# Performance work log

Hardware: AMD Instinct MI355X
Metric: run time of the kernel (lower is better)

## Reference

```python
import jax, jax.numpy as jnp
import numpy as np

EMBED = 1024
HEADS = 16
HEAD_DIM = EMBED // HEADS
MAX_REL = 8
B, S = 4, 1024


def setup_inputs() -> dict:
    key = jax.random.key(0)
    ks = jax.random.split(key, 12)
    lim = 1.0 / np.sqrt(EMBED)
    def lin(k):
        k1, k2 = jax.random.split(k)
        W = jax.random.uniform(k1, (EMBED, EMBED), jnp.float32, -lim, lim)
        b = jax.random.uniform(k2, (EMBED,), jnp.float32, -lim, lim)
        return W, b
    Wq, bq = lin(ks[0]); Wk, bk = lin(ks[1]); Wv, bv = lin(ks[2]); Wo, bo = lin(ks[3])
    return {
        'query': jax.random.normal(ks[4], (B, S, EMBED), jnp.float32),
        'key': jax.random.normal(ks[5], (B, S, EMBED), jnp.float32),
        'value': jax.random.normal(ks[6], (B, S, EMBED), jnp.float32),
        'mask': jnp.zeros((B, S, S), dtype=bool),
        'Wq': Wq, 'bq': bq, 'Wk': Wk, 'bk': bk, 'Wv': Wv, 'bv': bv,
        'Wo': Wo, 'bo': bo,
        'rel_bias': jnp.zeros((HEADS, 2 * MAX_REL + 1), jnp.float32),
    }


def _split_heads(x):
    b, s, _ = x.shape
    return x.reshape(b, s, HEADS, HEAD_DIM).transpose(0, 2, 1, 3)  # [b,h,s,d]


def reference(query, key, value, mask, Wq, bq, Wk, bk, Wv, bv, Wo, bo, rel_bias):
    scale = jnp.sqrt(jnp.float32(HEAD_DIM))
    Q = _split_heads(query @ Wq.T + bq)
    K = _split_heads(key @ Wk.T + bk)
    V = _split_heads(value @ Wv.T + bv)
    scores = jnp.einsum('bhqd,bhkd->bhqk', Q, K) / scale
    # relative position bias: rel_bias[h, clip(j-i)+max]
    idx = jnp.arange(query.shape[1])
    rel = jnp.clip(idx[None, :] - idx[:, None], -MAX_REL, MAX_REL) + MAX_REL  # [s,s]
    bias = rel_bias[:, rel]  # [h,s,s]
    scores = scores + bias[None]
    scores = jnp.where(mask[:, None, :, :], -jnp.inf, scores)
    attn = jax.nn.softmax(scores, axis=-1)
    ctx = jnp.einsum('bhqk,bhkd->bhqd', attn, V)
    b, h, s, d = ctx.shape
    out = ctx.transpose(0, 2, 1, 3).reshape(b, s, h * d) @ Wo.T + bo
    return out, attn, scores
```

## Files before the change

### kernel.cpp

```cpp
#include <hip/hip_runtime.h>

typedef __bf16 bf16_t;
typedef bf16_t bf16x4 __attribute__((ext_vector_type(4)));
typedef bf16_t bf16x8 __attribute__((ext_vector_type(8)));
typedef float f32x4 __attribute__((ext_vector_type(4)));
typedef float f32x8 __attribute__((ext_vector_type(8)));

#define B_N 4
#define S_N 1024
#define E_N 1024
#define H_N 16
#define D_N 64

#define MFMA16 __builtin_amdgcn_mfma_f32_16x16x32_bf16

static __device__ __forceinline__ bf16_t f2b(float x) { return (bf16_t)x; }

static __device__ __forceinline__ void gload_lds16(const void* g, void* l) {
  __builtin_amdgcn_global_load_lds(
      (const __attribute__((address_space(1))) unsigned int*)g,
      (__attribute__((address_space(3))) unsigned int*)l, 16, 0, 0);
}

static __device__ __forceinline__ void lds_barrier() {
  asm volatile("s_waitcnt lgkmcnt(0)\n\ts_barrier" ::: "memory");
  __builtin_amdgcn_sched_barrier(0);
}

__global__ __launch_bounds__(256) void convert_kernel(
    const float* __restrict__ q, const float* __restrict__ k, const float* __restrict__ v,
    const float* __restrict__ wq, const float* __restrict__ wk,
    const float* __restrict__ wv, const float* __restrict__ wo,
    bf16_t* __restrict__ dq, bf16_t* __restrict__ dk, bf16_t* __restrict__ dv,
    bf16_t* __restrict__ dwq, bf16_t* __restrict__ dwk,
    bf16_t* __restrict__ dwv, bf16_t* __restrict__ dwo)
{
  const size_t e = ((size_t)blockIdx.x * 256 + threadIdx.x) * 8;
  const float* src; bf16_t* dst; size_t off;
  if (e < 12582912ull) {
    const int which = (int)(e >> 22);
    off = e & 4194303ull;
    src = which == 0 ? q : (which == 1 ? k : v);
    dst = which == 0 ? dq : (which == 1 ? dk : dv);
  } else {
    const size_t e2 = e - 12582912ull;
    const int which = (int)(e2 >> 20);
    off = e2 & 1048575ull;
    src = which == 0 ? wq : (which == 1 ? wk : (which == 2 ? wv : wo));
    dst = which == 0 ? dwq : (which == 1 ? dwk : (which == 2 ? dwv : dwo));
  }
  f32x8 x = *(const f32x8*)(src + off);
  bf16x8 r;
#pragma unroll
  for (int i = 0; i < 8; ++i) r[i] = f2b(x[i]);
  *(bf16x8*)(dst + off) = r;
}

__global__ __launch_bounds__(256) void mask_rowany(
    const unsigned char* __restrict__ mask, unsigned char* __restrict__ flags)
{
  const int row = blockIdx.x * 4 + (threadIdx.x >> 6);
  const int lane = threadIdx.x & 63;
  const uint4 v = *(const uint4*)(mask + (size_t)row * 1024 + lane * 16);
  const unsigned int any = v.x | v.y | v.z | v.w;
  const unsigned long long bal = __ballot(any != 0);
  if (lane == 0) flags[row] = bal ? 1 : 0;
}

__global__ __launch_bounds__(256) void qkv_gemm(
    const bf16_t* __restrict__ qA, const bf16_t* __restrict__ kA, const bf16_t* __restrict__ vA,
    const bf16_t* __restrict__ Wq, const bf16_t* __restrict__ Wk, const bf16_t* __restrict__ Wv,
    const float* __restrict__ bq, const float* __restrict__ bk, const float* __restrict__ bv,
    bf16_t* __restrict__ Qo, bf16_t* __restrict__ Ko, bf16_t* __restrict__ Vto)
{
  const int z = blockIdx.z;
  const bf16_t* A = z == 0 ? qA : (z == 1 ? kA : vA);
  const bf16_t* W = z == 0 ? Wq : (z == 1 ? Wk : Wv);
  const float* bias = z == 0 ? bq : (z == 1 ? bk : bv);

  __shared__ bf16_t As[128 * 32];
  __shared__ bf16_t Bs[128 * 32];
  const int tid = threadIdx.x;
  const int m0 = blockIdx.y * 128, n0 = blockIdx.x * 128;
  const int lane = tid & 63, wid = tid >> 6;
  const int wr = wid >> 1, wc = wid & 1;
  const int lr = lane & 15, lh = lane >> 4;
  const int sr = lane >> 2, sc = (lane & 3) * 8;
  f32x4 acc[4][4] = {};
  for (int k0 = 0; k0 < 1024; k0 += 32) {
#pragma unroll
    for (int i = 0; i < 2; ++i) {
      const int br = wid * 32 + i * 16;
      gload_lds16(&A[(size_t)(m0 + br + sr) * 1024 + k0 + sc], &As[br * 32]);
      gload_lds16(&W[(size_t)(n0 + br + sr) * 1024 + k0 + sc], &Bs[br * 32]);
    }
    __syncthreads();
    bf16x8 af[4], bw[4];
#pragma unroll
    for (int m = 0; m < 4; ++m)
      af[m] = *(const bf16x8*)&As[(wr * 64 + m * 16 + lr) * 32 + lh * 8];
#pragma unroll
    for (int n = 0; n < 4; ++n)
      bw[n] = *(const bf16x8*)&Bs[(wc * 64 + n * 16 + lr) * 32 + lh * 8];
#pragma unroll
    for (int m = 0; m < 4; ++m)
#pragma unroll
      for (int n = 0; n < 4; ++n)
        acc[m][n] = MFMA16(af[m], bw[n], acc[m][n], 0, 0, 0);
    __syncthreads();
  }
#pragma unroll
  for (int n = 0; n < 4; ++n) {
    const int col = n0 + wc * 64 + n * 16 + lr;
    const float bv_ = bias[col];
    const int h = col >> 6, d = col & 63;
#pragma unroll
    for (int m = 0; m < 4; ++m) {
      const int row0 = m0 + wr * 64 + m * 16 + lh * 4;
#pragma unroll
      for (int r = 0; r < 4; ++r) {
        const int row = row0 + r;
        const float v = acc[m][n][r] + bv_;
        const int b = row >> 10, s = row & 1023;
        if (z == 0)
          Qo[((size_t)(b * H_N + h) * S_N + s) * D_N + d] = f2b(v);
        else if (z == 1)
          Ko[((size_t)(b * H_N + h) * S_N + s) * D_N + d] = f2b(v);
        else
          Vto[((size_t)(b * H_N + h) * D_N + d) * S_N + s] = f2b(v);
      }
    }
  }
}

__global__ __launch_bounds__(256) void out_gemm(
    const bf16_t* __restrict__ A, const bf16_t* __restrict__ W,
    const float* __restrict__ bias, float* __restrict__ Co)
{
  __shared__ bf16_t As[128 * 32];
  __shared__ bf16_t Bs[128 * 32];
  const int tid = threadIdx.x;
  const int m0 = blockIdx.y * 128, n0 = blockIdx.x * 128;
  const int lane = tid & 63, wid = tid >> 6;
  const int wr = wid >> 1, wc = wid & 1;
  const int lr = lane & 15, lh = lane >> 4;
  const int sr = lane >> 2, sc = (lane & 3) * 8;
  f32x4 acc[4][4] = {};
  for (int k0 = 0; k0 < 1024; k0 += 32) {
#pragma unroll
    for (int i = 0; i < 2; ++i) {
      const int br = wid * 32 + i * 16;
      gload_lds16(&A[(size_t)(m0 + br + sr) * 1024 + k0 + sc], &As[br * 32]);
      gload_lds16(&W[(size_t)(n0 + br + sr) * 1024 + k0 + sc], &Bs[br * 32]);
    }
    __syncthreads();
    bf16x8 af[4], bw[4];
#pragma unroll
    for (int m = 0; m < 4; ++m)
      af[m] = *(const bf16x8*)&As[(wr * 64 + m * 16 + lr) * 32 + lh * 8];
#pragma unroll
    for (int n = 0; n < 4; ++n)
      bw[n] = *(const bf16x8*)&Bs[(wc * 64 + n * 16 + lr) * 32 + lh * 8];
#pragma unroll
    for (int m = 0; m < 4; ++m)
#pragma unroll
      for (int n = 0; n < 4; ++n)
        acc[m][n] = MFMA16(af[m], bw[n], acc[m][n], 0, 0, 0);
    __syncthreads();
  }
#pragma unroll
  for (int n = 0; n < 4; ++n) {
    const int col = n0 + wc * 64 + n * 16 + lr;
    const float bv_ = bias[col];
#pragma unroll
    for (int m = 0; m < 4; ++m) {
      const int row0 = m0 + wr * 64 + m * 16 + lh * 4;
#pragma unroll
      for (int r = 0; r < 4; ++r)
        Co[(size_t)(row0 + r) * E_N + col] = acc[m][n][r] + bv_;
    }
  }
}

static __device__ __forceinline__ f32x4 score4(
    f32x4 acc, int qrow, int kc, const unsigned char* __restrict__ mrow,
    const float* __restrict__ rbh, float rb_lo, float rb_hi, bool um)
{
  const int d0 = kc - qrow;
  float b0, b1, b2, b3;
  if (d0 >= 8) { b0 = b1 = b2 = b3 = rb_hi; }
  else if (d0 <= -11) { b0 = b1 = b2 = b3 = rb_lo; }
  else {
    int dd;
    dd = d0;     dd = dd < -8 ? -8 : (dd > 8 ? 8 : dd); b0 = rbh[dd + 8];
    dd = d0 + 1; dd = dd < -8 ? -8 : (dd > 8 ? 8 : dd); b1 = rbh[dd + 8];
    dd = d0 + 2; dd = dd < -8 ? -8 : (dd > 8 ? 8 : dd); b2 = rbh[dd + 8];
    dd = d0 + 3; dd = dd < -8 ? -8 : (dd > 8 ? 8 : dd); b3 = rbh[dd + 8];
  }
  f32x4 s;
  s[0] = acc[0] * 0.125f + b0;
  s[1] = acc[1] * 0.125f + b1;
  s[2] = acc[2] * 0.125f + b2;
  s[3] = acc[3] * 0.125f + b3;
  if (um) {
    const unsigned int mw = *(const unsigned int*)(mrow + kc);
    const float NEG = -__builtin_inff();
    if (mw & 0xffu)       s[0] = NEG;
    if (mw & 0xff00u)     s[1] = NEG;
    if (mw & 0xff0000u)   s[2] = NEG;
    if (mw & 0xff000000u) s[3] = NEG;
  }
  return s;
}

__global__ __launch_bounds__(512) void fused_attn(
    const bf16_t* __restrict__ Q, const bf16_t* __restrict__ K,
    const bf16_t* __restrict__ Vt,
    const unsigned char* __restrict__ mask, const unsigned char* __restrict__ rowflag,
    const float* __restrict__ rel_bias,
    float* __restrict__ scores, float* __restrict__ attn, bf16_t* __restrict__ ctx)
{
  __shared__ bf16_t Ktile[2][64 * 64];
  __shared__ bf16_t Vtile[2][64 * 64];
  __shared__ float S_lds[8][16][68];

  int flat = blockIdx.y * 4 + blockIdx.x;
  flat = (flat & 7) * 64 + (flat >> 3);
  const int bh = flat >> 3, b = bh >> 4, h = bh & 15;
  const int q0 = (flat & 7) * 128;

  const int tid = threadIdx.x;
  const int w = tid >> 6, lane = tid & 63;
  const int lr = lane & 15, lh = lane >> 4;
  const int qrow = q0 + w * 16 + lr;

  const bf16_t* Qh = Q + (size_t)bh * (S_N * D_N);
  const bf16_t* Kh = K + (size_t)bh * (S_N * D_N);
  const bf16_t* Vh = Vt + (size_t)bh * (D_N * S_N);
  const unsigned char* mrow = mask + (size_t)b * S_N * S_N + (size_t)qrow * S_N;
  float* Sbase = scores + (size_t)bh * S_N * S_N + (size_t)(q0 + w * 16) * S_N;
  float* Abase = attn + (size_t)bh * S_N * S_N + (size_t)(q0 + w * 16) * S_N;
  const float* rbh = rel_bias + h * 17;
  const float rb_lo = rbh[0], rb_hi = rbh[16];
  const float NEG = -__builtin_inff();
  const float THR = 8.0f;
  const bool um = rowflag[b * S_N + qrow] != 0;

  const int sg_row = tid >> 3, sg_c = tid & 7;
  const int sg_s = (sg_c ^ (sg_row & 7)) * 8;

  bf16x8 qa0 = *(const bf16x8*)&Qh[(size_t)qrow * D_N + lh * 8];
  bf16x8 qa1 = *(const bf16x8*)&Qh[(size_t)qrow * D_N + 32 + lh * 8];

  const int ks0 = (lh ^ (lr & 7)) * 8;
  const int ks1 = ((4 + lh) ^ (lr & 7)) * 8;

  float mrun = NEG, srun = 0.f;
  *(bf16x8*)&Ktile[0][sg_row * 64 + sg_s] =
      *(const bf16x8*)&Kh[(size_t)sg_row * D_N + sg_c * 8];
  lds_barrier();
  for (int kt = 0; kt < 16; ++kt) {
    const int cur = kt & 1, kb = kt * 64;
    bf16x8 krn;
    if (kt + 1 < 16)
      krn = *(const bf16x8*)&Kh[(size_t)(kb + 64 + sg_row) * D_N + sg_c * 8];
    f32x4 sr4[4];
    float mloc = NEG;
#pragma unroll
    for (int t = 0; t < 4; ++t) {
      const int krow = t * 16 + lr;
      bf16x8 ka0 = *(const bf16x8*)&Ktile[cur][krow * 64 + ks0];
      bf16x8 ka1 = *(const bf16x8*)&Ktile[cur][krow * 64 + ks1];
      f32x4 acc = {};
      acc = MFMA16(ka0, qa0, acc, 0, 0, 0);
      acc = MFMA16(ka1, qa1, acc, 0, 0, 0);
      const int kc = kb + t * 16 + 4 * lh;
      f32x4 s = score4(acc, qrow, kc, mrow, rbh, rb_lo, rb_hi, um);
      sr4[t] = s;
      *(f32x4*)&S_lds[w][lr][t * 16 + 4 * lh] = s;
      mloc = fmaxf(mloc, fmaxf(fmaxf(s[0], s[1]), fmaxf(s[2], s[3])));
    }
    mloc = fmaxf(mloc, __shfl_xor(mloc, 16));
    mloc = fmaxf(mloc, __shfl_xor(mloc, 32));
    if (__any(mloc - mrun > THR)) {
      const float mn = fmaxf(mrun, mloc);
      if (mn > NEG) {
        srun = srun * __expf(mrun - mn);
        mrun = mn;
      }
    }
    const bool live = mrun > NEG;
    float ls = 0.f;
#pragma unroll
    for (int t = 0; t < 4; ++t) {
      f32x4 s = sr4[t];
      float e0 = live ? __expf(s[0] - mrun) : 0.f;
      float e1 = live ? __expf(s[1] - mrun) : 0.f;
      float e2 = live ? __expf(s[2] - mrun) : 0.f;
      float e3 = live ? __expf(s[3] - mrun) : 0.f;
      ls += (e0 + e1) + (e2 + e3);
    }
    srun += ls;
#pragma unroll
    for (int i = 0; i < 4; ++i) {
      const int row = 4 * i + lh;
      f32x4 sv = *(const f32x4*)&S_lds[w][row][lr * 4];
      __builtin_nontemporal_store(sv, (f32x4*)&Sbase[(size_t)row * S_N + kb + lr * 4]);
    }
    if (kt + 1 < 16)
      *(bf16x8*)&Ktile[cur ^ 1][sg_row * 64 + sg_s] = krn;
    lds_barrier();
  }
  srun += __shfl_xor(srun, 16);
  srun += __shfl_xor(srun, 32);
  const float M = mrun;
  const float invs = 1.0f / srun;

  f32x4 accp[4] = {};
  *(bf16x8*)&Ktile[0][sg_row * 64 + sg_s] =
      *(const bf16x8*)&Kh[(size_t)sg_row * D_N + sg_c * 8];
  *(bf16x8*)&Vtile[0][sg_row * 64 + sg_s] =
      *(const bf16x8*)&Vh[(size_t)sg_row * S_N + sg_c * 8];
  lds_barrier();
  for (int kt = 0; kt < 16; ++kt) {
    const int cur = kt & 1, kb = kt * 64;
    bf16x8 krn, vrn;
    if (kt + 1 < 16) {
      krn = *(const bf16x8*)&Kh[(size_t)(kb + 64 + sg_row) * D_N + sg_c * 8];
      vrn = *(const bf16x8*)&Vh[(size_t)sg_row * S_N + kb + 64 + sg_c * 8];
    }
#pragma unroll
    for (int t = 0; t < 4; ++t) {
      const int krow = t * 16 + lr;
      bf16x8 ka0 = *(const bf16x8*)&Ktile[cur][krow * 64 + ks0];
      bf16x8 ka1 = *(const bf16x8*)&Ktile[cur][krow * 64 + ks1];
      f32x4 acc = {};
      acc = MFMA16(ka0, qa0, acc, 0, 0, 0);
      acc = MFMA16(ka1, qa1, acc, 0, 0, 0);
      const int kc = kb + t * 16 + 4 * lh;
      f32x4 s = score4(acc, qrow, kc, mrow, rbh, rb_lo, rb_hi, um);
      f32x4 p;
#pragma unroll
      for (int j = 0; j < 4; ++j) p[j] = __expf(s[j] - M) * invs;
      *(f32x4*)&S_lds[w][lr][t * 16 + 4 * lh] = p;
    }
#pragma unroll
    for (int i = 0; i < 4; ++i) {
      const int row = 4 * i + lh;
      f32x4 pv = *(const f32x4*)&S_lds[w][row][lr * 4];
      __builtin_nontemporal_store(pv, (f32x4*)&Abase[(size_t)row * S_N + kb + lr * 4]);
    }
#pragma unroll
    for (int ch = 0; ch < 2; ++ch) {
      f32x8 pf = *(const f32x8*)&S_lds[w][lr][ch * 32 + lh * 8];
      bf16x8 pa;
#pragma unroll
      for (int j = 0; j < 8; ++j) pa[j] = f2b(pf[j]);
#pragma unroll
      for (int dt = 0; dt < 4; ++dt) {
        const int drow = dt * 16 + lr;
        bf16x8 vb = *(const bf16x8*)&Vtile[cur][drow * 64 + (((ch * 4 + lh) ^ (lr & 7)) * 8)];
        accp[dt] = MFMA16(pa, vb, accp[dt], 0, 0, 0);
      }
    }
    if (kt + 1 < 16) {
      *(bf16x8*)&Ktile[cur ^ 1][sg_row * 64 + sg_s] = krn;
      *(bf16x8*)&Vtile[cur ^ 1][sg_row * 64 + sg_s] = vrn;
    }
    lds_barrier();
  }
#pragma unroll
  for (int dt = 0; dt < 4; ++dt)
#pragma unroll
    for (int r = 0; r < 4; ++r)
      ctx[((size_t)(b * S_N + q0 + w * 16 + 4 * lh + r)) * E_N + h * 64 + dt * 16 + lr] =
          f2b(accp[dt][r]);
}

extern "C" void kernel_launch(void* const* d_in, const int* in_sizes, int n_in,
                              void* d_out, int out_size, void* d_ws, size_t ws_size,
                              hipStream_t stream) {
  (void)in_sizes; (void)n_in; (void)out_size; (void)ws_size;
  const float* query = (const float*)d_in[0];
  const float* key   = (const float*)d_in[1];
  const float* value = (const float*)d_in[2];
  const unsigned char* mask = (const unsigned char*)d_in[3];
  const float* Wq = (const float*)d_in[4];
  const float* bq = (const float*)d_in[5];
  const float* Wk = (const float*)d_in[6];
  const float* bk = (const float*)d_in[7];
  const float* Wv = (const float*)d_in[8];
  const float* bv = (const float*)d_in[9];
  const float* Wo = (const float*)d_in[10];
  const float* bo = (const float*)d_in[11];
  const float* rel_bias = (const float*)d_in[12];

  float* out_f    = (float*)d_out;
  float* attn_f   = out_f + (size_t)4194304;
  float* scores_f = attn_f + (size_t)67108864;

  char* ws = (char*)d_ws;
  bf16_t* qbf  = (bf16_t*)(ws);
  bf16_t* kbf  = (bf16_t*)(ws + (8ull  << 20));
  bf16_t* vbf  = (bf16_t*)(ws + (16ull << 20));
  bf16_t* Wqb  = (bf16_t*)(ws + (24ull << 20));
  bf16_t* Wkb  = (bf16_t*)(ws + (26ull << 20));
  bf16_t* Wvb  = (bf16_t*)(ws + (28ull << 20));
  bf16_t* Wob  = (bf16_t*)(ws + (30ull << 20));
  bf16_t* Qbf  = (bf16_t*)(ws + (32ull << 20));
  bf16_t* Kbf  = (bf16_t*)(ws + (40ull << 20));
  bf16_t* Vtbf = (bf16_t*)(ws + (48ull << 20));
  bf16_t* CTX  = (bf16_t*)(ws + (56ull << 20));
  unsigned char* FLAGS = (unsigned char*)(ws + (64ull << 20));

  convert_kernel<<<dim3(8192), dim3(256), 0, stream>>>(
      query, key, value, Wq, Wk, Wv, Wo, qbf, kbf, vbf, Wqb, Wkb, Wvb, Wob);
  mask_rowany<<<dim3(1024), dim3(256), 0, stream>>>(mask, FLAGS);
  qkv_gemm<<<dim3(8, 32, 3), dim3(256), 0, stream>>>(
      qbf, kbf, vbf, Wqb, Wkb, Wvb, bq, bk, bv, Qbf, Kbf, Vtbf);
  fused_attn<<<dim3(4, 128), dim3(512), 0, stream>>>(
      Qbf, Kbf, Vtbf, mask, FLAGS, rel_bias, scores_f, attn_f, CTX);
  out_gemm<<<dim3(8, 32), dim3(256), 0, stream>>>(CTX, Wob, bo, out_f);
}
```

Baseline: 214.6 us.

## Fuse activation fp32-to-bf16 conversion into QKV GEMM and merge mask-flag kernel

The QKV GEMM now loads the fp32 query/key/value activations directly, converts them to bf16 in registers and stores them into shared memory. This removes the separate pass that wrote bf16 copies of the activations to a workspace and read them back. The mask row-any flag computation is folded into the weight conversion kernel, saving one launch. In exchange, the A operand loses the async global-to-LDS load and is re-read in fp32 by each of the 8 column blocks, doubling the bytes fetched per A tile.

Measured after the change: 224.5 us. 1.05x slower.

```diff
diff --git a/kernel.cpp b/kernel.cpp
--- a/kernel.cpp
+++ b/kernel.cpp
@@ -27,28 +27,27 @@
   __builtin_amdgcn_sched_barrier(0);
 }
 
-__global__ __launch_bounds__(256) void convert_kernel(
-    const float* __restrict__ q, const float* __restrict__ k, const float* __restrict__ v,
+__global__ __launch_bounds__(256) void convert_mask_kernel(
     const float* __restrict__ wq, const float* __restrict__ wk,
     const float* __restrict__ wv, const float* __restrict__ wo,
-    bf16_t* __restrict__ dq, bf16_t* __restrict__ dk, bf16_t* __restrict__ dv,
     bf16_t* __restrict__ dwq, bf16_t* __restrict__ dwk,
-    bf16_t* __restrict__ dwv, bf16_t* __restrict__ dwo)
+    bf16_t* __restrict__ dwv, bf16_t* __restrict__ dwo,
+    const unsigned char* __restrict__ mask, unsigned char* __restrict__ flags)
 {
+  if (blockIdx.x >= 2048) {
+    const int row = (blockIdx.x - 2048) * 4 + (threadIdx.x >> 6);
+    const int lane = threadIdx.x & 63;
+    const uint4 mv = *(const uint4*)(mask + (size_t)row * 1024 + lane * 16);
+    const unsigned int any = mv.x | mv.y | mv.z | mv.w;
+    const unsigned long long bal = __ballot(any != 0);
+    if (lane == 0) flags[row] = bal ? 1 : 0;
+    return;
+  }
   const size_t e = ((size_t)blockIdx.x * 256 + threadIdx.x) * 8;
-  const float* src; bf16_t* dst; size_t off;
-  if (e < 12582912ull) {
-    const int which = (int)(e >> 22);
-    off = e & 4194303ull;
-    src = which == 0 ? q : (which == 1 ? k : v);
-    dst = which == 0 ? dq : (which == 1 ? dk : dv);
-  } else {
-    const size_t e2 = e - 12582912ull;
-    const int which = (int)(e2 >> 20);
-    off = e2 & 1048575ull;
-    src = which == 0 ? wq : (which == 1 ? wk : (which == 2 ? wv : wo));
-    dst = which == 0 ? dwq : (which == 1 ? dwk : (which == 2 ? dwv : dwo));
-  }
+  const int which = (int)(e >> 20);
+  const size_t off = e & 1048575ull;
+  const float* src = which == 0 ? wq : (which == 1 ? wk : (which == 2 ? wv : wo));
+  bf16_t* dst = which == 0 ? dwq : (which == 1 ? dwk : (which == 2 ? dwv : dwo));
   f32x8 x = *(const f32x8*)(src + off);
   bf16x8 r;
 #pragma unroll
@@ -56,25 +55,14 @@
   *(bf16x8*)(dst + off) = r;
 }
 
-__global__ __launch_bounds__(256) void mask_rowany(
-    const unsigned char* __restrict__ mask, unsigned char* __restrict__ flags)
-{
-  const int row = blockIdx.x * 4 + (threadIdx.x >> 6);
-  const int lane = threadIdx.x & 63;
-  const uint4 v = *(const uint4*)(mask + (size_t)row * 1024 + lane * 16);
-  const unsigned int any = v.x | v.y | v.z | v.w;
-  const unsigned long long bal = __ballot(any != 0);
-  if (lane == 0) flags[row] = bal ? 1 : 0;
-}
-
 __global__ __launch_bounds__(256) void qkv_gemm(
-    const bf16_t* __restrict__ qA, const bf16_t* __restrict__ kA, const bf16_t* __restrict__ vA,
+    const float* __restrict__ qA, const float* __restrict__ kA, const float* __restrict__ vA,
     const bf16_t* __restrict__ Wq, const bf16_t* __restrict__ Wk, const bf16_t* __restrict__ Wv,
     const float* __restrict__ bq, const float* __restrict__ bk, const float* __restrict__ bv,
     bf16_t* __restrict__ Qo, bf16_t* __restrict__ Ko, bf16_t* __restrict__ Vto)
 {
   const int z = blockIdx.z;
-  const bf16_t* A = z == 0 ? qA : (z == 1 ? kA : vA);
+  const float* A = z == 0 ? qA : (z == 1 ? kA : vA);
   const bf16_t* W = z == 0 ? Wq : (z == 1 ? Wk : Wv);
   const float* bias = z == 0 ? bq : (z == 1 ? bk : bv);
 
@@ -86,14 +74,21 @@
   const int wr = wid >> 1, wc = wid & 1;
   const int lr = lane & 15, lh = lane >> 4;
   const int sr = lane >> 2, sc = (lane & 3) * 8;
+  const int ar = tid >> 2, ac = (tid & 3) * 8;
   f32x4 acc[4][4] = {};
   for (int k0 = 0; k0 < 1024; k0 += 32) {
+    f32x8 a0 = *(const f32x8*)&A[(size_t)(m0 + ar) * 1024 + k0 + ac];
+    f32x8 a1 = *(const f32x8*)&A[(size_t)(m0 + ar + 64) * 1024 + k0 + ac];
 #pragma unroll
     for (int i = 0; i < 2; ++i) {
       const int br = wid * 32 + i * 16;
-      gload_lds16(&A[(size_t)(m0 + br + sr) * 1024 + k0 + sc], &As[br * 32]);
       gload_lds16(&W[(size_t)(n0 + br + sr) * 1024 + k0 + sc], &Bs[br * 32]);
     }
+    bf16x8 b0, b1;
+#pragma unroll
+    for (int i = 0; i < 8; ++i) { b0[i] = f2b(a0[i]); b1[i] = f2b(a1[i]); }
+    *(bf16x8*)&As[ar * 32 + ac] = b0;
+    *(bf16x8*)&As[(ar + 64) * 32 + ac] = b1;
     __syncthreads();
     bf16x8 af[4], bw[4];
 #pragma unroll
@@ -400,24 +395,20 @@
   float* scores_f = attn_f + (size_t)67108864;
 
   char* ws = (char*)d_ws;
-  bf16_t* qbf  = (bf16_t*)(ws);
-  bf16_t* kbf  = (bf16_t*)(ws + (8ull  << 20));
-  bf16_t* vbf  = (bf16_t*)(ws + (16ull << 20));
-  bf16_t* Wqb  = (bf16_t*)(ws + (24ull << 20));
-  bf16_t* Wkb  = (bf16_t*)(ws + (26ull << 20));
-  bf16_t* Wvb  = (bf16_t*)(ws + (28ull << 20));
-  bf16_t* Wob  = (bf16_t*)(ws + (30ull << 20));
-  bf16_t* Qbf  = (bf16_t*)(ws + (32ull << 20));
-  bf16_t* Kbf  = (bf16_t*)(ws + (40ull << 20));
-  bf16_t* Vtbf = (bf16_t*)(ws + (48ull << 20));
-  bf16_t* CTX  = (bf16_t*)(ws + (56ull << 20));
-  unsigned char* FLAGS = (unsigned char*)(ws + (64ull << 20));
-
-  convert_kernel<<<dim3(8192), dim3(256), 0, stream>>>(
-      query, key, value, Wq, Wk, Wv, Wo, qbf, kbf, vbf, Wqb, Wkb, Wvb, Wob);
-  mask_rowany<<<dim3(1024), dim3(256), 0, stream>>>(mask, FLAGS);
+  bf16_t* Wqb  = (bf16_t*)(ws);
+  bf16_t* Wkb  = (bf16_t*)(ws + (2ull  << 20));
+  bf16_t* Wvb  = (bf16_t*)(ws + (4ull  << 20));
+  bf16_t* Wob  = (bf16_t*)(ws + (6ull  << 20));
+  bf16_t* Qbf  = (bf16_t*)(ws + (8ull  << 20));
+  bf16_t* Kbf  = (bf16_t*)(ws + (16ull << 20));
+  bf16_t* Vtbf = (bf16_t*)(ws + (24ull << 20));
+  bf16_t* CTX  = (bf16_t*)(ws + (32ull << 20));
+  unsigned char* FLAGS = (unsigned char*)(ws + (40ull << 20));
+
+  convert_mask_kernel<<<dim3(3072), dim3(256), 0, stream>>>(
+      Wq, Wk, Wv, Wo, Wqb, Wkb, Wvb, Wob, mask, FLAGS);
   qkv_gemm<<<dim3(8, 32, 3), dim3(256), 0, stream>>>(
-      qbf, kbf, vbf, Wqb, Wkb, Wvb, bq, bk, bv, Qbf, Kbf, Vtbf);
+      query, key, value, Wqb, Wkb, Wvb, bq, bk, bv, Qbf, Kbf, Vtbf);
   fused_attn<<<dim3(4, 128), dim3(512), 0, stream>>>(
       Qbf, Kbf, Vtbf, mask, FLAGS, rel_bias, scores_f, attn_f, CTX);
   out_gemm<<<dim3(8, 32), dim3(256), 0, stream>>>(CTX, Wob, bo, out_f);
```
